# Kernel tuning notes

Hardware: AMD Instinct MI355X
Metric: run time of the kernel (lower is better)

The kernel has to match this reference:

```python
import jax, jax.numpy as jnp
import numpy as np

# Dims
B, C, H, W = 16, 64, 64, 64
EXPAND, D_CONV, D_STATE = 2, 4, 16
D_INNER = EXPAND * C            # 128
DT_RANK = (C + 15) // 16        # ceil(64/16) = 4
LEAK = 0.01


def leaky_relu(x):
    return jnp.where(x >= 0, x, LEAK * x)


def conv2d_3x3(x, w, b):
    # x: [B,C,H,W], w: [C,C,3,3]
    y = jax.lax.conv_general_dilated(x, w, (1, 1), ((1, 1), (1, 1)),
                                     dimension_numbers=('NCHW', 'OIHW', 'NCHW'))
    return y + b[None, :, None, None]


def mamba(xseq, in_proj_w, conv1d_w, conv1d_b, x_proj_w, dt_proj_w, dt_proj_b, A_log, D, out_proj_w):
    # xseq: [B, L, C]
    bN, L, _ = xseq.shape
    xz = xseq @ in_proj_w                      # [B,L,2*d_inner]
    x, z = jnp.split(xz, 2, axis=-1)           # each [B,L,d_inner]
    # causal depthwise conv1d along L
    k = conv1d_w.shape[-1]
    xc = jnp.transpose(x, (0, 2, 1))           # [B,d_inner,L]
    xc = jnp.pad(xc, ((0, 0), (0, 0), (k - 1, 0)))
    xc = jax.lax.conv_general_dilated(xc, conv1d_w, (1,), 'VALID',
                                      dimension_numbers=('NCH', 'OIH', 'NCH'),
                                      feature_group_count=D_INNER)
    x = jax.nn.silu(jnp.transpose(xc + conv1d_b[None, :, None], (0, 2, 1)))  # [B,L,d_inner]
    # input-dependent SSM params
    dbc = x @ x_proj_w                         # [B,L,dt_rank+2*d_state]
    dt = dbc[..., :DT_RANK]
    Bm = dbc[..., DT_RANK:DT_RANK + D_STATE]   # [B,L,N]
    Cm = dbc[..., DT_RANK + D_STATE:]          # [B,L,N]
    delta = jax.nn.softplus(dt @ dt_proj_w + dt_proj_b)  # [B,L,d_inner]
    A = -jnp.exp(A_log)                        # [d_inner,N]

    def step(h, inp):
        d_t, u_t, b_t, c_t = inp               # [B,d],[B,d],[B,N],[B,N]
        h = jnp.exp(d_t[..., None] * A) * h + (d_t * u_t)[..., None] * b_t[:, None, :]
        y = jnp.einsum('bdn,bn->bd', h, c_t)
        return h, y

    h0 = jnp.zeros((bN, D_INNER, D_STATE), xseq.dtype)
    xs = (jnp.moveaxis(delta, 1, 0), jnp.moveaxis(x, 1, 0),
          jnp.moveaxis(Bm, 1, 0), jnp.moveaxis(Cm, 1, 0))
    _, ys = jax.lax.scan(step, h0, xs)         # ys: [L,B,d_inner]
    y = jnp.moveaxis(ys, 0, 1) + x * D         # skip via D
    y = y * jax.nn.silu(z)                     # gated
    return y @ out_proj_w                      # [B,L,C]


def setup_inputs() -> dict:
    key = jax.random.key(0)
    ks = jax.random.split(key, 14)
    s = 0.02
    inp = {
        'x': jax.random.normal(ks[0], (B, C, H, W), jnp.float32),
        'conv_w1': jax.random.normal(ks[1], (C, C, 3, 3), jnp.float32) * s,
        'conv_b1': jnp.zeros((C,), jnp.float32),
        'conv_w2': jax.random.normal(ks[2], (C, C, 3, 3), jnp.float32) * s,
        'conv_b2': jnp.zeros((C,), jnp.float32),
        'in_proj_w': jax.random.normal(ks[3], (C, 2 * D_INNER), jnp.float32) * s,
        'conv1d_w': jax.random.normal(ks[4], (D_INNER, 1, D_CONV), jnp.float32) * s,
        'conv1d_b': jnp.zeros((D_INNER,), jnp.float32),
        'x_proj_w': jax.random.normal(ks[5], (D_INNER, DT_RANK + 2 * D_STATE), jnp.float32) * s,
        'dt_proj_w': jax.random.normal(ks[6], (DT_RANK, D_INNER), jnp.float32) * s,
        'dt_proj_b': jnp.full((D_INNER,), -4.0, jnp.float32),  # softplus(-4) ~ small dt
        'A_log': jnp.log(jnp.tile(jnp.arange(1, D_STATE + 1, dtype=jnp.float32), (D_INNER, 1))),
        'D': jnp.ones((D_INNER,), jnp.float32),
        'out_proj_w': jax.random.normal(ks[7], (D_INNER, C), jnp.float32) * s,
    }
    return inp


def reference(x, conv_w1, conv_b1, conv_w2, conv_b2, in_proj_w, conv1d_w, conv1d_b,
              x_proj_w, dt_proj_w, dt_proj_b, A_log, D, out_proj_w):
    bN, cN, hN, wN = x.shape
    y = leaky_relu(conv2d_3x3(x, conv_w1, conv_b1))
    y = leaky_relu(conv2d_3x3(y, conv_w2, conv_b2))
    seq = y.reshape(bN, cN, hN * wN).transpose(0, 2, 1)   # [B,L,C]
    seq = mamba(seq, in_proj_w, conv1d_w, conv1d_b, x_proj_w,
                dt_proj_w, dt_proj_b, A_log, D, out_proj_w)
    return seq.transpose(0, 2, 1).reshape(bN, cN, hN, wN)
```

## Files before the change

kernel.cpp:

```cpp
#include <hip/hip_runtime.h>
#include <math.h>

#define NB   16
#define NCH  64
#define NH   64
#define NW   64
#define NL   4096
#define DIN  128
#define DST  16
#define DTR  4
#define NJ   256
#define NCHK 128
#define CT   32
#define NCHK3 128
#define CT3  32

#define RSZ 8388608ull

#define EXP2(x) __builtin_amdgcn_exp2f(x)

typedef _Float16 f16x8 __attribute__((ext_vector_type(8)));
typedef float    f32x4 __attribute__((ext_vector_type(4)));

__global__ void k_prep(const float* __restrict__ w1, const float* __restrict__ w2,
                       const float* __restrict__ alog, const float* __restrict__ wout,
                       _Float16* __restrict__ wf1, _Float16* __restrict__ wf2,
                       _Float16* __restrict__ wt16, float* __restrict__ A1) {
  int i = blockIdx.x * 256 + threadIdx.x;
  if (i < 9 * 64 * 64) {
    int t  = i >> 12;
    int co = (i >> 6) & 63;
    int ci = i & 63;
    wf1[i] = (_Float16)w1[(co * 64 + ci) * 9 + t];
    wf2[i] = (_Float16)w2[(co * 64 + ci) * 9 + t];
  }
  if (i < 64 * 128) {
    int c = i >> 7, d = i & 127;
    wt16[i] = (_Float16)wout[d * 64 + c];
  }
  if (i < DIN * DST) A1[i] = -__expf(alog[i]) * 1.44269504088896f;
}

__global__ __launch_bounds__(256, 2) void k_convmfma(
    const float* __restrict__ in, const _Float16* __restrict__ Wf,
    const float* __restrict__ bias, float* __restrict__ out) {
  __shared__ __align__(16) _Float16 xs[4][66][72];
  const int tid  = threadIdx.x;
  const int wv   = tid >> 6;
  const int lane = tid & 63;
  const int b    = blockIdx.y;
  const int h0   = blockIdx.x * 2;

  {
    const int rr = wv;
    const int h  = h0 - 1 + rr;
    const bool ok = (h >= 0) && (h < NH);
    for (int ci = 0; ci < NCH; ++ci) {
      float v = ok ? in[(((size_t)b * NCH + ci) * NH + h) * NW + lane] : 0.f;
      xs[rr][lane + 1][ci] = (_Float16)v;
      if (lane < 2) xs[rr][lane ? 65 : 0][ci] = (_Float16)0.f;
    }
  }
  __syncthreads();

  const int r      = wv & 1;
  const int cohalf = wv >> 1;
  const int kgrp   = lane >> 4;
  const int ln16   = lane & 15;

  f32x4 acc[2][4];
#pragma unroll
  for (int m = 0; m < 2; ++m)
#pragma unroll
    for (int f = 0; f < 4; ++f) acc[m][f] = (f32x4){0.f, 0.f, 0.f, 0.f};

  const _Float16* wbase = Wf + (size_t)(cohalf * 32 + ln16) * 64 + kgrp * 8;

#pragma unroll
  for (int ts = 0; ts < 18; ++ts) {
    const int t  = ts >> 1;
    const int s  = ts & 1;
    const int kh = t / 3;
    const int kw = t - kh * 3;
    f16x8 af[2];
#pragma unroll
    for (int m = 0; m < 2; ++m)
      af[m] = *(const f16x8*)(wbase + ((size_t)t * 64 + m * 16) * 64 + s * 32);
    f16x8 bf[4];
#pragma unroll
    for (int f = 0; f < 4; ++f)
      bf[f] = *(const f16x8*)&xs[r + kh][16 * f + kw + ln16][s * 32 + kgrp * 8];
#pragma unroll
    for (int m = 0; m < 2; ++m)
#pragma unroll
      for (int f = 0; f < 4; ++f)
        acc[m][f] = __builtin_amdgcn_mfma_f32_16x16x32_f16(af[m], bf[f],
                                                           acc[m][f], 0, 0, 0);
  }

  float bv[2][4];
#pragma unroll
  for (int m = 0; m < 2; ++m)
#pragma unroll
    for (int reg = 0; reg < 4; ++reg)
      bv[m][reg] = bias[cohalf * 32 + m * 16 + kgrp * 4 + reg];
#pragma unroll
  for (int m = 0; m < 2; ++m) {
    const int cob = cohalf * 32 + m * 16 + kgrp * 4;
#pragma unroll
    for (int f = 0; f < 4; ++f) {
#pragma unroll
      for (int reg = 0; reg < 4; ++reg) {
        float v = acc[m][f][reg] + bv[m][reg];
        v = v >= 0.f ? v : 0.01f * v;
        out[(((size_t)b * NCH + cob + reg) * NH + h0 + r) * NW + 16 * f + ln16] = v;
      }
    }
  }
}

__global__ __launch_bounds__(256) void k_inproj(
    const float* __restrict__ Y, const float* __restrict__ Win,
    float* __restrict__ xpre, float* __restrict__ z) {
  const int tid  = threadIdx.x;
  const int wv   = __builtin_amdgcn_readfirstlane(tid >> 6);
  const int lane = tid & 63;
  const int b    = blockIdx.z;
  const int l    = blockIdx.x * 64 + lane;
  const int j0   = blockIdx.y * 64 + wv * 16;
  const float* yp = Y + (size_t)b * NCH * NL + l;
  const float* wp = Win + j0;
  float acc[16];
#pragma unroll
  for (int j = 0; j < 16; ++j) acc[j] = 0.f;
  for (int c = 0; c < NCH; ++c) {
    const float yv = yp[(size_t)c * NL];
    const float* w = wp + c * NJ;
#pragma unroll
    for (int j = 0; j < 16; ++j) acc[j] = fmaf(yv, w[j], acc[j]);
  }
  float* outp = (j0 < DIN)
      ? (xpre + ((size_t)b * NL + l) * DIN + j0)
      : (z + ((size_t)b * NL + l) * DIN + (j0 - DIN));
#pragma unroll
  for (int j4 = 0; j4 < 4; ++j4)
    *(float4*)&outp[j4 * 4] = make_float4(acc[j4 * 4 + 0], acc[j4 * 4 + 1],
                                          acc[j4 * 4 + 2], acc[j4 * 4 + 3]);
}

__global__ void k_dwconv(const float* __restrict__ xpre,
                         const float* __restrict__ w1d,
                         const float* __restrict__ b1d,
                         float* __restrict__ u) {
  const int gid = blockIdx.x * 256 + threadIdx.x;
  const int d4  = gid & 31;
  const int bl  = gid >> 5;
  const int l   = bl & (NL - 1);
  const int d0  = d4 * 4;
  const float* xp = xpre + (size_t)bl * DIN + d0;
  float4 xk[4];
#pragma unroll
  for (int k = 0; k < 4; ++k) {
    const int lk = l - 3 + k;
    xk[k] = (lk >= 0) ? *(const float4*)&xp[(k - 3) * DIN]
                      : make_float4(0.f, 0.f, 0.f, 0.f);
  }
  float4 o;
  float* po = (float*)&o;
#pragma unroll
  for (int p = 0; p < 4; ++p) {
    const int d = d0 + p;
    float v = b1d[d];
    v = fmaf(w1d[d * 4 + 0], ((const float*)&xk[0])[p], v);
    v = fmaf(w1d[d * 4 + 1], ((const float*)&xk[1])[p], v);
    v = fmaf(w1d[d * 4 + 2], ((const float*)&xk[2])[p], v);
    v = fmaf(w1d[d * 4 + 3], ((const float*)&xk[3])[p], v);
    po[p] = __fdividef(v, 1.f + __expf(-v));
  }
  *(float4*)&u[(size_t)bl * DIN + d0] = o;
}

__global__ __launch_bounds__(256) void k_xproj(
    const float* __restrict__ u, const float* __restrict__ Wxp,
    const float* __restrict__ Wdt, const float* __restrict__ bdt,
    float* __restrict__ BmT, float* __restrict__ CmT,
    float* __restrict__ delta) {
  __shared__ float ut[64][129];
  __shared__ float dbcs[64][37];
  const int tid  = threadIdx.x;
  const int wv   = __builtin_amdgcn_readfirstlane(tid >> 6);
  const int lane = tid & 63;
  const size_t g0 = (size_t)blockIdx.x * 64;

#pragma unroll
  for (int pass = 0; pass < 8; ++pass) {
    const int f   = pass * 256 + tid;
    const int row = f >> 5;
    const int c4  = f & 31;
    const float4 v = *(const float4*)&u[(g0 + row) * DIN + c4 * 4];
    ut[row][c4 * 4 + 0] = v.x;
    ut[row][c4 * 4 + 1] = v.y;
    ut[row][c4 * 4 + 2] = v.z;
    ut[row][c4 * 4 + 3] = v.w;
  }
  __syncthreads();

  {
    const int j0 = wv * 9;
    float acc[9];
#pragma unroll
    for (int j = 0; j < 9; ++j) acc[j] = 0.f;
    const float* wx = Wxp + j0;
#pragma unroll 4
    for (int d = 0; d < DIN; ++d) {
      const float uu = ut[lane][d];
      const float* w = wx + d * 36;
#pragma unroll
      for (int j = 0; j < 9; ++j) acc[j] = fmaf(uu, w[j], acc[j]);
    }
#pragma unroll
    for (int j = 0; j < 9; ++j) dbcs[lane][j0 + j] = acc[j];
  }
  __syncthreads();

  const float dt0 = dbcs[lane][0], dt1 = dbcs[lane][1];
  const float dt2 = dbcs[lane][2], dt3 = dbcs[lane][3];

  if (wv == 0) {
    float* bp = BmT + (g0 + lane) * 16;
#pragma unroll
    for (int n4 = 0; n4 < 4; ++n4)
      *(float4*)&bp[n4 * 4] =
          make_float4(dbcs[lane][4 + n4 * 4 + 0], dbcs[lane][4 + n4 * 4 + 1],
                      dbcs[lane][4 + n4 * 4 + 2], dbcs[lane][4 + n4 * 4 + 3]);
  } else if (wv == 1) {
    float* cp = CmT + (g0 + lane) * 16;
#pragma unroll
    for (int n4 = 0; n4 < 4; ++n4)
      *(float4*)&cp[n4 * 4] =
          make_float4(dbcs[lane][20 + n4 * 4 + 0], dbcs[lane][20 + n4 * 4 + 1],
                      dbcs[lane][20 + n4 * 4 + 2], dbcs[lane][20 + n4 * 4 + 3]);
  }
  __syncthreads();

  {
    const int d0 = wv * 32;
#pragma unroll 4
    for (int k = 0; k < 32; ++k) {
      const int d = d0 + k;
      float s = bdt[d];
      s = fmaf(dt0, Wdt[0 * DIN + d], s);
      s = fmaf(dt1, Wdt[1 * DIN + d], s);
      s = fmaf(dt2, Wdt[2 * DIN + d], s);
      s = fmaf(dt3, Wdt[3 * DIN + d], s);
      ut[lane][d] = fmaxf(s, 0.f) + __logf(1.f + __expf(-fabsf(s)));
    }
  }
  __syncthreads();

#pragma unroll
  for (int pass = 0; pass < 8; ++pass) {
    const int f   = pass * 256 + tid;
    const int row = f >> 5;
    const int c4  = f & 31;
    float4 v;
    v.x = ut[row][c4 * 4 + 0];
    v.y = ut[row][c4 * 4 + 1];
    v.z = ut[row][c4 * 4 + 2];
    v.w = ut[row][c4 * 4 + 3];
    *(float4*)&delta[(g0 + row) * DIN + c4 * 4] = v;
  }
}

__global__ __launch_bounds__(128) void k_scan1(
    const float* __restrict__ delta, const float* __restrict__ u,
    const float* __restrict__ BmT, const float* __restrict__ A1,
    float* __restrict__ P, float* __restrict__ Q) {
  const int d  = threadIdx.x;
  const int b  = blockIdx.y;
  const int ck = blockIdx.x;
  const int t0 = ck * CT;
  const float* dp = delta + ((size_t)b * NL + t0) * DIN + d;
  const float* up = u + ((size_t)b * NL + t0) * DIN + d;
  const float* bp = BmT + ((size_t)b * NL + t0) * 16;
  float a1[DST], Pr[DST], Qr[DST];
#pragma unroll
  for (int n = 0; n < 16; n += 4) {
    float4 t = *(const float4*)&A1[d * 16 + n];
    a1[n] = t.x; a1[n + 1] = t.y; a1[n + 2] = t.z; a1[n + 3] = t.w;
  }
#pragma unroll
  for (int n = 0; n < 16; ++n) { Pr[n] = 1.f; Qr[n] = 0.f; }

  auto grp = [&](const float* ld, const float* lu, int tb) {
#pragma unroll
    for (int q = 0; q < 4; ++q) {
      const float db = ld[q] * lu[q];
      const float* br = bp + (tb + q) * 16;
#pragma unroll
      for (int n = 0; n < 16; ++n) {
        const float a = EXP2(ld[q] * a1[n]);
        Pr[n] *= a;
        Qr[n] = fmaf(a, Qr[n], db * br[n]);
      }
    }
  };

  float ldA[4], luA[4], ldB[4], luB[4];
#pragma unroll
  for (int q = 0; q < 4; ++q) {
    ldA[q] = dp[(size_t)q * DIN];
    luA[q] = up[(size_t)q * DIN];
  }
  for (int tt = 0; tt < CT; tt += 8) {
#pragma unroll
    for (int q = 0; q < 4; ++q) {
      ldB[q] = dp[(size_t)(tt + 4 + q) * DIN];
      luB[q] = up[(size_t)(tt + 4 + q) * DIN];
    }
    grp(ldA, luA, tt);
    if (tt < CT - 8) {
#pragma unroll
      for (int q = 0; q < 4; ++q) {
        ldA[q] = dp[(size_t)(tt + 8 + q) * DIN];
        luA[q] = up[(size_t)(tt + 8 + q) * DIN];
      }
    }
    grp(ldB, luB, tt + 4);
  }

  const size_t o = (((size_t)b * NCHK + ck) * DIN + d) * 16;
#pragma unroll
  for (int n4 = 0; n4 < 4; ++n4) {
    *(float4*)&P[o + n4 * 4] = make_float4(Pr[n4 * 4], Pr[n4 * 4 + 1],
                                           Pr[n4 * 4 + 2], Pr[n4 * 4 + 3]);
    *(float4*)&Q[o + n4 * 4] = make_float4(Qr[n4 * 4], Qr[n4 * 4 + 1],
                                           Qr[n4 * 4 + 2], Qr[n4 * 4 + 3]);
  }
}

__global__ __launch_bounds__(256) void k_scan2(
    const float* __restrict__ P, const float* __restrict__ Q,
    float* __restrict__ H0) {
  const int tid = threadIdx.x;
  const int b   = blockIdx.y;
  const int d   = blockIdx.x * 16 + (tid >> 4);
  const int n   = tid & 15;
  const size_t base = ((size_t)b * NCHK * DIN + d) * 16 + n;
  const size_t cs   = (size_t)DIN * 16;
  const float* pp = P + base;
  const float* qp = Q + base;
  float* hp = H0 + base;
  float h = 0.f;
  for (int c = 0; c < NCHK; c += 8) {
    float pv[8], qv[8];
#pragma unroll
    for (int k = 0; k < 8; ++k) {
      pv[k] = pp[k * cs];
      qv[k] = qp[k * cs];
    }
#pragma unroll
    for (int k = 0; k < 8; ++k) {
      hp[k * cs] = h;
      h = fmaf(pv[k], h, qv[k]);
    }
    pp += 8 * cs; qp += 8 * cs; hp += 8 * cs;
  }
}

__global__ __launch_bounds__(128) void k_scan3(
    const float* __restrict__ delta, const float* __restrict__ u,
    const float* __restrict__ zb, const float* __restrict__ BmT,
    const float* __restrict__ CmT, const float* __restrict__ A1,
    const float* __restrict__ H0, const float* __restrict__ Dvec,
    const _Float16* __restrict__ Wt16, float* __restrict__ out) {
  __shared__ __align__(16) _Float16 yyT[CT3][DIN + 8];
  const int d  = threadIdx.x;
  const int b  = blockIdx.y;
  const int ck = blockIdx.x;
  const int t0 = ck * CT3;
  const float* dp = delta + ((size_t)b * NL + t0) * DIN + d;
  const float* up = u + ((size_t)b * NL + t0) * DIN + d;
  const float* zp = zb + ((size_t)b * NL + t0) * DIN + d;
  const float* bp = BmT + ((size_t)b * NL + t0) * 16;
  const float* cp = CmT + ((size_t)b * NL + t0) * 16;
  float a1[DST], h[DST];
  {
    const size_t ho = (((size_t)b * NCHK + ck) * DIN + d) * 16;
#pragma unroll
    for (int n = 0; n < 16; n += 4) {
      float4 t = *(const float4*)&A1[d * 16 + n];
      a1[n] = t.x; a1[n + 1] = t.y; a1[n + 2] = t.z; a1[n + 3] = t.w;
      float4 hv = *(const float4*)&H0[ho + n];
      h[n] = hv.x; h[n + 1] = hv.y; h[n + 2] = hv.z; h[n + 3] = hv.w;
    }
  }
  const float Dd = Dvec[d];

  auto grp = [&](const float* ld4, const float* lu4, const float* lz4, int tb) {
#pragma unroll
    for (int q = 0; q < 4; ++q) {
      const float ld = ld4[q], lu = lu4[q], lz = lz4[q];
      const float db = ld * lu;
      const float* br = bp + (tb + q) * 16;
      const float* cr = cp + (tb + q) * 16;
      float y0 = 0.f, y1 = 0.f, y2 = 0.f, y3 = 0.f;
#pragma unroll
      for (int n = 0; n < 16; n += 4) {
        const float e0 = EXP2(ld * a1[n + 0]);
        const float e1 = EXP2(ld * a1[n + 1]);
        const float e2 = EXP2(ld * a1[n + 2]);
        const float e3 = EXP2(ld * a1[n + 3]);
        h[n + 0] = fmaf(e0, h[n + 0], db * br[n + 0]);
        h[n + 1] = fmaf(e1, h[n + 1], db * br[n + 1]);
        h[n + 2] = fmaf(e2, h[n + 2], db * br[n + 2]);
        h[n + 3] = fmaf(e3, h[n + 3], db * br[n + 3]);
        y0 = fmaf(h[n + 0], cr[n + 0], y0);
        y1 = fmaf(h[n + 1], cr[n + 1], y1);
        y2 = fmaf(h[n + 2], cr[n + 2], y2);
        y3 = fmaf(h[n + 3], cr[n + 3], y3);
      }
      const float yt = fmaf(lu, Dd, (y0 + y1) + (y2 + y3));
      const float sz = __fdividef(lz, 1.f + __expf(-lz));
      yyT[tb + q][d] = (_Float16)(yt * sz);
    }
  };

  float ldA[4], luA[4], lzA[4], ldB[4], luB[4], lzB[4];
#pragma unroll
  for (int q = 0; q < 4; ++q) {
    ldA[q] = dp[(size_t)q * DIN];
    luA[q] = up[(size_t)q * DIN];
    lzA[q] = zp[(size_t)q * DIN];
  }
  for (int tt = 0; tt < CT3; tt += 8) {
#pragma unroll
    for (int q = 0; q < 4; ++q) {
      ldB[q] = dp[(size_t)(tt + 4 + q) * DIN];
      luB[q] = up[(size_t)(tt + 4 + q) * DIN];
      lzB[q] = zp[(size_t)(tt + 4 + q) * DIN];
    }
    grp(ldA, luA, lzA, tt);
    if (tt < CT3 - 8) {
#pragma unroll
      for (int q = 0; q < 4; ++q) {
        ldA[q] = dp[(size_t)(tt + 8 + q) * DIN];
        luA[q] = up[(size_t)(tt + 8 + q) * DIN];
        lzA[q] = zp[(size_t)(tt + 8 + q) * DIN];
      }
    }
    grp(ldB, luB, lzB, tt + 4);
  }
  __syncthreads();

  const int wv   = d >> 6;
  const int lane = d & 63;
  const int kgrp = lane >> 4;
  const int ln16 = lane & 15;
  f32x4 acc[4];
#pragma unroll
  for (int m = 0; m < 4; ++m) acc[m] = (f32x4){0.f, 0.f, 0.f, 0.f};
#pragma unroll
  for (int ks = 0; ks < 4; ++ks) {
    const f16x8 bf = *(const f16x8*)&yyT[wv * 16 + ln16][ks * 32 + kgrp * 8];
#pragma unroll
    for (int m = 0; m < 4; ++m) {
      const f16x8 af =
          *(const f16x8*)&Wt16[(size_t)(m * 16 + ln16) * 128 + ks * 32 + kgrp * 8];
      acc[m] = __builtin_amdgcn_mfma_f32_16x16x32_f16(af, bf, acc[m], 0, 0, 0);
    }
  }
#pragma unroll
  for (int m = 0; m < 4; ++m) {
    const int col = wv * 16 + ln16;
#pragma unroll
    for (int reg = 0; reg < 4; ++reg) {
      const int c = m * 16 + kgrp * 4 + reg;
      out[((size_t)b * NCH + c) * NL + t0 + col] = acc[m][reg];
    }
  }
}

extern "C" void kernel_launch(void* const* d_in, const int* in_sizes, int n_in,
                              void* d_out, int out_size, void* d_ws,
                              size_t ws_size, hipStream_t stream) {
  (void)in_sizes; (void)n_in; (void)out_size; (void)ws_size;
  const float* x    = (const float*)d_in[0];
  const float* w1   = (const float*)d_in[1];
  const float* b1   = (const float*)d_in[2];
  const float* w2   = (const float*)d_in[3];
  const float* b2   = (const float*)d_in[4];
  const float* win  = (const float*)d_in[5];
  const float* w1d  = (const float*)d_in[6];
  const float* b1d  = (const float*)d_in[7];
  const float* wxp  = (const float*)d_in[8];
  const float* wdt  = (const float*)d_in[9];
  const float* bdt  = (const float*)d_in[10];
  const float* alog = (const float*)d_in[11];
  const float* dvec = (const float*)d_in[12];
  const float* wout = (const float*)d_in[13];
  float* out = (float*)d_out;
  float* ws  = (float*)d_ws;

  float* c1   = ws;
  float* dl   = ws;
  float* c2   = ws + RSZ;
  float* bmt  = ws + RSZ;
  float* cmt  = ws + RSZ + 1048576;
  float* Pb   = ws + RSZ + 2097152;
  float* xpre = ws + 2 * RSZ;
  float* Qb   = ws + 2 * RSZ;
  float* H0b  = ws + 2 * RSZ + 4194304;
  float* zbuf = ws + 3 * RSZ;
  float* ubuf = ws + 4 * RSZ;
  float* Ab   = ws + 5 * RSZ;
  _Float16* wf1  = (_Float16*)(Ab + 2048);
  _Float16* wf2  = wf1 + 9 * 64 * 64;
  _Float16* wt16 = wf2 + 9 * 64 * 64;

  k_prep<<<144, 256, 0, stream>>>(w1, w2, alog, wout, wf1, wf2, wt16, Ab);
  k_convmfma<<<dim3(32, 16), 256, 0, stream>>>(x, wf1, b1, c1);
  k_convmfma<<<dim3(32, 16), 256, 0, stream>>>(c1, wf2, b2, c2);
  k_inproj<<<dim3(64, 4, 16), 256, 0, stream>>>(c2, win, xpre, zbuf);
  k_dwconv<<<8192, 256, 0, stream>>>(xpre, w1d, b1d, ubuf);
  k_xproj<<<1024, 256, 0, stream>>>(ubuf, wxp, wdt, bdt, bmt, cmt, dl);
  k_scan1<<<dim3(NCHK, NB), 128, 0, stream>>>(dl, ubuf, bmt, Ab, Pb, Qb);
  k_scan2<<<dim3(8, NB), 256, 0, stream>>>(Pb, Qb, H0b);
  k_scan3<<<dim3(NCHK3, NB), 128, 0, stream>>>(dl, ubuf, zbuf, bmt, cmt, Ab,
                                               H0b, dvec, wt16, out);
}
```

Before: 243.4 us.

## Widen conv blocks to 8 waves and re-tile in_proj over positions

The 3x3 MFMA conv now runs 512 threads per block. Each wave computes one 16-output-channel slice instead of two, and the shared-memory staging is split across waves by channel half, written as packed 8-wide f16 stores. The in_proj GEMM is re-tiled so each lane owns 4 output columns and each wave 16 sequence positions. Weights become coalesced float4 loads, while activations are read as uniform per-wave scalars. This raises parallelism and store width, but the conv's per-wave input reuse is halved and the in_proj grid has fewer blocks.

```diff
diff --git a/kernel.cpp b/kernel.cpp
--- a/kernel.cpp
+++ b/kernel.cpp
@@ -41,7 +41,7 @@
   if (i < DIN * DST) A1[i] = -__expf(alog[i]) * 1.44269504088896f;
 }
 
-__global__ __launch_bounds__(256, 2) void k_convmfma(
+__global__ __launch_bounds__(512, 4) void k_convmfma(
     const float* __restrict__ in, const _Float16* __restrict__ Wf,
     const float* __restrict__ bias, float* __restrict__ out) {
   __shared__ __align__(16) _Float16 xs[4][66][72];
@@ -52,29 +52,43 @@
   const int h0   = blockIdx.x * 2;
 
   {
-    const int rr = wv;
-    const int h  = h0 - 1 + rr;
+    const int rr  = wv >> 1;
+    const int ci0 = (wv & 1) * 32;
+    const int h   = h0 - 1 + rr;
     const bool ok = (h >= 0) && (h < NH);
-    for (int ci = 0; ci < NCH; ++ci) {
-      float v = ok ? in[(((size_t)b * NCH + ci) * NH + h) * NW + lane] : 0.f;
-      xs[rr][lane + 1][ci] = (_Float16)v;
-      if (lane < 2) xs[rr][lane ? 65 : 0][ci] = (_Float16)0.f;
+    const float* ip = in + (((size_t)b * NCH + ci0) * NH + h) * NW + lane;
+#pragma unroll
+    for (int oct = 0; oct < 4; ++oct) {
+      _Float16 pk[8];
+#pragma unroll
+      for (int k = 0; k < 8; ++k) {
+        const float v = ok ? ip[(size_t)(oct * 8 + k) * (NH * NW)] : 0.f;
+        pk[k] = (_Float16)v;
+      }
+      *(f16x8*)&xs[rr][lane + 1][ci0 + oct * 8] = *(const f16x8*)pk;
+    }
+    if (lane < 2) {
+      const int col = lane ? 65 : 0;
+      _Float16 zz[8];
+#pragma unroll
+      for (int k = 0; k < 8; ++k) zz[k] = (_Float16)0.f;
+#pragma unroll
+      for (int oct = 0; oct < 4; ++oct)
+        *(f16x8*)&xs[rr][col][ci0 + oct * 8] = *(const f16x8*)zz;
     }
   }
   __syncthreads();
 
-  const int r      = wv & 1;
-  const int cohalf = wv >> 1;
-  const int kgrp   = lane >> 4;
-  const int ln16   = lane & 15;
-
-  f32x4 acc[2][4];
-#pragma unroll
-  for (int m = 0; m < 2; ++m)
-#pragma unroll
-    for (int f = 0; f < 4; ++f) acc[m][f] = (f32x4){0.f, 0.f, 0.f, 0.f};
-
-  const _Float16* wbase = Wf + (size_t)(cohalf * 32 + ln16) * 64 + kgrp * 8;
+  const int r    = wv & 1;
+  const int coq  = wv >> 1;
+  const int kgrp = lane >> 4;
+  const int ln16 = lane & 15;
+
+  f32x4 acc[4];
+#pragma unroll
+  for (int f = 0; f < 4; ++f) acc[f] = (f32x4){0.f, 0.f, 0.f, 0.f};
+
+  const _Float16* wbase = Wf + (size_t)(coq * 16 + ln16) * 64 + kgrp * 8;
 
 #pragma unroll
   for (int ts = 0; ts < 18; ++ts) {
@@ -82,70 +96,66 @@
     const int s  = ts & 1;
     const int kh = t / 3;
     const int kw = t - kh * 3;
-    f16x8 af[2];
-#pragma unroll
-    for (int m = 0; m < 2; ++m)
-      af[m] = *(const f16x8*)(wbase + ((size_t)t * 64 + m * 16) * 64 + s * 32);
+    const f16x8 af = *(const f16x8*)(wbase + (size_t)t * 4096 + s * 32);
     f16x8 bf[4];
 #pragma unroll
     for (int f = 0; f < 4; ++f)
       bf[f] = *(const f16x8*)&xs[r + kh][16 * f + kw + ln16][s * 32 + kgrp * 8];
 #pragma unroll
-    for (int m = 0; m < 2; ++m)
-#pragma unroll
-      for (int f = 0; f < 4; ++f)
-        acc[m][f] = __builtin_amdgcn_mfma_f32_16x16x32_f16(af[m], bf[f],
-                                                           acc[m][f], 0, 0, 0);
-  }
-
-  float bv[2][4];
-#pragma unroll
-  for (int m = 0; m < 2; ++m)
-#pragma unroll
-    for (int reg = 0; reg < 4; ++reg)
-      bv[m][reg] = bias[cohalf * 32 + m * 16 + kgrp * 4 + reg];
-#pragma unroll
-  for (int m = 0; m < 2; ++m) {
-    const int cob = cohalf * 32 + m * 16 + kgrp * 4;
-#pragma unroll
-    for (int f = 0; f < 4; ++f) {
-#pragma unroll
-      for (int reg = 0; reg < 4; ++reg) {
-        float v = acc[m][f][reg] + bv[m][reg];
-        v = v >= 0.f ? v : 0.01f * v;
-        out[(((size_t)b * NCH + cob + reg) * NH + h0 + r) * NW + 16 * f + ln16] = v;
-      }
-    }
-  }
-}
-
-__global__ __launch_bounds__(256) void k_inproj(
+    for (int f = 0; f < 4; ++f)
+      acc[f] = __builtin_amdgcn_mfma_f32_16x16x32_f16(af, bf[f], acc[f], 0, 0, 0);
+  }
+
+  float bv[4];
+#pragma unroll
+  for (int reg = 0; reg < 4; ++reg)
+    bv[reg] = bias[coq * 16 + kgrp * 4 + reg];
+#pragma unroll
+  for (int f = 0; f < 4; ++f) {
+#pragma unroll
+    for (int reg = 0; reg < 4; ++reg) {
+      const int co = coq * 16 + kgrp * 4 + reg;
+      float v = acc[f][reg] + bv[reg];
+      v = v >= 0.f ? v : 0.01f * v;
+      out[(((size_t)b * NCH + co) * NH + h0 + r) * NW + 16 * f + ln16] = v;
+    }
+  }
+}
+
+__global__ __launch_bounds__(256, 4) void k_inproj(
     const float* __restrict__ Y, const float* __restrict__ Win,
     float* __restrict__ xpre, float* __restrict__ z) {
   const int tid  = threadIdx.x;
   const int wv   = __builtin_amdgcn_readfirstlane(tid >> 6);
   const int lane = tid & 63;
-  const int b    = blockIdx.z;
-  const int l    = blockIdx.x * 64 + lane;
-  const int j0   = blockIdx.y * 64 + wv * 16;
-  const float* yp = Y + (size_t)b * NCH * NL + l;
-  const float* wp = Win + j0;
-  float acc[16];
-#pragma unroll
-  for (int j = 0; j < 16; ++j) acc[j] = 0.f;
+  const int b    = blockIdx.y;
+  const int l0   = blockIdx.x * 64 + wv * 16;
+  const int j0   = lane * 4;
+
+  float4 acc[16];
+#pragma unroll
+  for (int i = 0; i < 16; ++i) acc[i] = make_float4(0.f, 0.f, 0.f, 0.f);
+
+  const float* yp = Y + (size_t)b * NCH * NL + l0;
   for (int c = 0; c < NCH; ++c) {
-    const float yv = yp[(size_t)c * NL];
-    const float* w = wp + c * NJ;
-#pragma unroll
-    for (int j = 0; j < 16; ++j) acc[j] = fmaf(yv, w[j], acc[j]);
-  }
+    const float4 w4 = *(const float4*)&Win[c * NJ + j0];
+    const float* yr = yp + (size_t)c * NL;
+#pragma unroll
+    for (int i = 0; i < 16; ++i) {
+      const float yv = yr[i];
+      acc[i].x = fmaf(yv, w4.x, acc[i].x);
+      acc[i].y = fmaf(yv, w4.y, acc[i].y);
+      acc[i].z = fmaf(yv, w4.z, acc[i].z);
+      acc[i].w = fmaf(yv, w4.w, acc[i].w);
+    }
+  }
+
   float* outp = (j0 < DIN)
-      ? (xpre + ((size_t)b * NL + l) * DIN + j0)
-      : (z + ((size_t)b * NL + l) * DIN + (j0 - DIN));
-#pragma unroll
-  for (int j4 = 0; j4 < 4; ++j4)
-    *(float4*)&outp[j4 * 4] = make_float4(acc[j4 * 4 + 0], acc[j4 * 4 + 1],
-                                          acc[j4 * 4 + 2], acc[j4 * 4 + 3]);
+      ? (xpre + ((size_t)b * NL + l0) * DIN + j0)
+      : (z + ((size_t)b * NL + l0) * DIN + (j0 - DIN));
+#pragma unroll
+  for (int i = 0; i < 16; ++i)
+    *(float4*)&outp[(size_t)i * DIN] = acc[i];
 }
 
 __global__ void k_dwconv(const float* __restrict__ xpre,
@@ -519,9 +529,9 @@
   _Float16* wt16 = wf2 + 9 * 64 * 64;
 
   k_prep<<<144, 256, 0, stream>>>(w1, w2, alog, wout, wf1, wf2, wt16, Ab);
-  k_convmfma<<<dim3(32, 16), 256, 0, stream>>>(x, wf1, b1, c1);
-  k_convmfma<<<dim3(32, 16), 256, 0, stream>>>(c1, wf2, b2, c2);
-  k_inproj<<<dim3(64, 4, 16), 256, 0, stream>>>(c2, win, xpre, zbuf);
+  k_convmfma<<<dim3(32, 16), 512, 0, stream>>>(x, wf1, b1, c1);
+  k_convmfma<<<dim3(32, 16), 512, 0, stream>>>(c1, wf2, b2, c2);
+  k_inproj<<<dim3(64, 16), 256, 0, stream>>>(c2, win, xpre, zbuf);
   k_dwconv<<<8192, 256, 0, stream>>>(xpre, w1d, b1d, ubuf);
   k_xproj<<<1024, 256, 0, stream>>>(ubuf, wxp, wdt, bdt, bmt, cmt, dl);
   k_scan1<<<dim3(NCHK, NB), 128, 0, stream>>>(dl, ubuf, bmt, Ab, Pb, Qb);
```

Measured after the change: 213.8 us. -12.2%, faster.
